# Performance work log

Hardware: AMD Instinct MI355X
Metric: run time of the kernel (lower is better)

Reference implementation:

```python
import jax, jax.numpy as jnp
import numpy as np

B, T, CIN, HID, OUT, H, W = 8, 8, 128, 64, 64, 32, 32


def _conv(x, w, b):
    # x: [B, C, H, W], w: [O, C, kh, kw] -> SAME-padded conv, stride 1
    y = jax.lax.conv_general_dilated(x, w, (1, 1), "SAME",
                                     dimension_numbers=("NCHW", "OIHW", "NCHW"))
    return y + b[None, :, None, None]


def _layer_dir(xs, w_ih, w_hh, b_ih, b_hh, reverse):
    # xs: [T, B, C, H, W]; one direction of a ConvLSTM layer; returns hs [T, B, HID, H, W]
    b, hh_, ww_ = xs.shape[1], xs.shape[3], xs.shape[4]
    h0 = jnp.zeros((b, HID, hh_, ww_), xs.dtype)

    def step(carry, x):
        h, c = carry
        gates = _conv(x, w_ih, b_ih) + _conv(h, w_hh, b_hh)  # [B, 4*HID, H, W]
        i, f, g, o = jnp.split(gates, 4, axis=1)
        c = jax.nn.sigmoid(f) * c + jax.nn.sigmoid(i) * jnp.tanh(g)
        h = jax.nn.sigmoid(o) * jnp.tanh(c)
        return (h, c), h

    _, hs = jax.lax.scan(step, (h0, h0), xs, reverse=reverse)
    return hs


def _forward(features, w_ih0f, w_hh0f, b_ih0f, b_hh0f,
             w_ih0r, w_hh0r, b_ih0r, b_hh0r,
             w_ih1f, w_hh1f, b_ih1f, b_hh1f,
             w_ih1r, w_hh1r, b_ih1r, b_hh1r,
             w_out, b_out):
    xs = jnp.transpose(features, (1, 0, 2, 3, 4))  # [T, B, C, H, W]
    # layer 0, both directions (scan reverse=True aligns outputs to original time order)
    hf = _layer_dir(xs, w_ih0f, w_hh0f, b_ih0f, b_hh0f, False)
    hr = _layer_dir(xs, w_ih0r, w_hh0r, b_ih0r, b_hh0r, True)
    xs1 = jnp.concatenate([hf, hr], axis=2)  # [T, B, 2*HID, H, W] (dropout is identity at eval)
    # layer 1
    hf1 = _layer_dir(xs1, w_ih1f, w_hh1f, b_ih1f, b_hh1f, False)
    hr1 = _layer_dir(xs1, w_ih1r, w_hh1r, b_ih1r, b_hh1r, True)
    last = jnp.concatenate([hf1[-1], hr1[-1]], axis=1)  # output[:, -1] -> [B, 2*HID, H, W]
    return jax.nn.relu(_conv(last, w_out, b_out))


def setup_inputs() -> dict:
    key = jax.random.key(0)
    ks = jax.random.split(key, 24)
    G = 4 * HID
    p = lambda k, s: jax.random.normal(k, s, jnp.float32) * 0.05
    d = {"features": jax.random.normal(ks[0], (B, T, CIN, H, W), jnp.float32)}
    i = 1
    for l, cin in ((0, CIN), (1, 2 * HID)):
        for dr in ("f", "r"):
            d[f"w_ih{l}{dr}"] = p(ks[i], (G, cin, 3, 3)); i += 1
            d[f"w_hh{l}{dr}"] = p(ks[i], (G, HID, 3, 3)); i += 1
            d[f"b_ih{l}{dr}"] = p(ks[i], (G,)); i += 1
            d[f"b_hh{l}{dr}"] = p(ks[i], (G,)); i += 1
    d["w_out"] = p(ks[i], (OUT, 2 * HID, 1, 1)); i += 1
    d["b_out"] = p(ks[i], (OUT,))
    return d


def reference(features, w_ih0f, w_hh0f, b_ih0f, b_hh0f,
              w_ih0r, w_hh0r, b_ih0r, b_hh0r,
              w_ih1f, w_hh1f, b_ih1f, b_hh1f,
              w_ih1r, w_hh1r, b_ih1r, b_hh1r,
              w_out, b_out):
    return _forward(features, w_ih0f, w_hh0f, b_ih0f, b_hh0f,
                    w_ih0r, w_hh0r, b_ih0r, b_hh0r,
                    w_ih1f, w_hh1f, b_ih1f, b_hh1f,
                    w_ih1r, w_hh1r, b_ih1r, b_hh1r,
                    w_out, b_out)
```

## Files before the change

kernel.cpp:

```cpp
#include <hip/hip_runtime.h>
#include <math.h>
#include <stdint.h>


typedef __attribute__((ext_vector_type(8))) short short8;
typedef __attribute__((ext_vector_type(4))) float float4v;

namespace {
constexpr int IMG = 34 * 34 * 64;
constexpr size_t SLOTI = 16ull * IMG;
constexpr int ROWB = 34 * 128;
constexpr int PADB = 8192;
}
template <int N> struct IC { static constexpr int v = N; };

__device__ __forceinline__ uint16_t bf16_rne(float x) {
  uint32_t u = __builtin_bit_cast(uint32_t, x);
  return (uint16_t)((u + 0x7FFFu + ((u >> 16) & 1u)) >> 16);
}
__device__ __forceinline__ float bf16_to_f(uint16_t h) {
  uint32_t u = ((uint32_t)h) << 16;
  return __builtin_bit_cast(float, u);
}

__device__ __forceinline__ void gl_lds16(const void* g, void* l) {
  __builtin_amdgcn_global_load_lds(
      (const __attribute__((address_space(1))) void*)g,
      (__attribute__((address_space(3))) void*)l, 16, 0, 0);
}

__global__ void pack_features(const float* __restrict__ f, uint16_t* __restrict__ out) {
  const size_t i = (size_t)blockIdx.x * 256 + threadIdx.x;
  const int blk_s = (int)(i & 7);
  size_t pp = i >> 3;
  const int px = (int)(pp % 34); pp /= 34;
  const int yy = (int)(pp % 34); pp /= 34;
  const int cg = (int)(pp & 3);
  const int bt = (int)(pp >> 2);
  const int b = bt & 7, t = bt >> 3;
  const int blk = blk_s ^ (px & 7);
  const int pl = blk >> 2, kg = blk & 3;
  short8 sv;
  if (px == 0 || px == 33 || yy == 0 || yy == 33) {
    #pragma unroll
    for (int j = 0; j < 8; ++j) sv[j] = 0;
  } else {
    const int x = px - 1, y = yy - 1;
    #pragma unroll
    for (int j = 0; j < 8; ++j) {
      const int ch = cg * 32 + kg * 8 + j;
      const float fv = f[(((size_t)b * 8 + t) * 128 + ch) * 1024 + y * 32 + x];
      const uint16_t hi = bf16_rne(fv);
      sv[j] = (short)(pl ? bf16_rne(fv - bf16_to_f(hi)) : hi);
    }
  }
  *(short8*)(out + i * 8) = sv;
}

struct WPackArgs {
  const float* wih[4]; const float* whh[4];
  const float* bih[4]; const float* bhh[4];
  uint32_t* wp; float* bp;
};
__global__ void pack_weights(WPackArgs A) {
  const int combo = blockIdx.y;
  const int idx = blockIdx.x * 256 + threadIdx.x;
  const int q = idx & 4095;
  const int rest = idx >> 12;
  const int nt = rest & 1;
  const int ct = rest >> 1;
  const int tap = ct % 9, cg = ct / 9;
  const int w2 = q & 3;
  const int b8s = (q >> 2) & 7;
  const int hcp = (q >> 5) & 15;
  const int g = (q >> 9) & 3;
  const int pl = (q >> 11) & 1;
  const int b8 = b8s ^ (hcp & 7);
  const int kg = b8 & 3;
  const int hcl = hcp * 2 + (b8 >> 2);
  const int n = g * 64 + nt * 32 + hcl;
  const float* wih = A.wih[combo];
  const float* whh = A.whh[combo];
  uint32_t out = 0;
  #pragma unroll
  for (int e = 0; e < 2; ++e) {
    const int ch = cg * 32 + kg * 8 + w2 * 2 + e;
    const float wv = (ch < 128) ? wih[((size_t)n * 128 + ch) * 9 + tap]
                                : whh[((size_t)n * 64 + (ch - 128)) * 9 + tap];
    const uint16_t hi = bf16_rne(wv);
    const uint16_t v = pl ? bf16_rne(wv - bf16_to_f(hi)) : hi;
    out |= ((uint32_t)v) << (16 * e);
  }
  A.wp[(size_t)combo * 442368 + idx] = out;
  if (idx < 256) A.bp[combo * 256 + idx] = A.bih[combo][idx] + A.bhh[combo][idx];
}

struct StepArgs {
  const uint16_t* in0; const uint16_t* in1; const uint16_t* in2;
  int nc0, nc1, nc2;
  const uint32_t* W;
  const float* bias;
  float* cbuf;
  uint16_t* himg;
  float* hf32;
};

__global__ __launch_bounds__(512, 2) void conv_lstm_step(StepArgs A0, StepArgs A1) {
  extern __shared__ char smem[];
  char* Asm_ = smem;
  char* Wsm_ = smem + 65536;

  const StepArgs a = (blockIdx.z == 0) ? A0 : A1;
  const int bx = blockIdx.x;
  const int nt = bx & 1;
  const int band = (bx >> 1) & 7;
  const int b = bx >> 4;
  const int y0 = band * 4;
  const int tid = threadIdx.x;
  const int lane = tid & 63;
  const int w = tid >> 6;
  const int m15 = lane & 15;
  const int kg = lane >> 4;
  const int r = w & 3;
  const int hcg = w >> 2;

  int offA[2][3][2];
  #pragma unroll
  for (int xh = 0; xh < 2; ++xh)
    #pragma unroll
    for (int kx = 0; kx < 3; ++kx)
      #pragma unroll
      for (int pl = 0; pl < 2; ++pl) {
        const int px = xh * 16 + kx + m15;
        const int sw = (pl * 4 + kg) ^ (px & 7);
        offA[xh][kx][pl] = r * ROWB + px * 128 + sw * 16;
      }
  int offW[2][4];
  {
    const int hcp = hcg * 8 + (m15 >> 1);
    const int b8 = kg + 4 * (m15 & 1);
    #pragma unroll
    for (int pl = 0; pl < 2; ++pl)
      #pragma unroll
      for (int g = 0; g < 4; ++g)
        offW[pl][g] = (((pl * 4 + g) * 16 + hcp) * 8 + (b8 ^ (hcp & 7))) * 16;
  }

  const int ncg = a.nc0 + a.nc1 + a.nc2;
  auto abase = [&](int cg) -> const char* {
    const uint16_t* t;
    if (cg < a.nc0) t = a.in0 + ((size_t)b * a.nc0 + cg) * IMG;
    else if (cg < a.nc0 + a.nc1) t = a.in1 + ((size_t)b * a.nc1 + (cg - a.nc0)) * IMG;
    else t = a.in2 + ((size_t)b * a.nc2 + (cg - a.nc0 - a.nc1)) * IMG;
    return (const char*)t + (size_t)y0 * ROWB;
  };
  auto stageA = [&](int cgi, int par) {
    const char* g = abase(cgi);
    char* d = Asm_ + par * 32768;
    #pragma unroll
    for (int j = 0; j < 4; ++j)
      gl_lds16(g + (size_t)(4 * w + j) * 1024 + lane * 16, d + (4 * w + j) * 1024);
  };
  auto stageW = [&](int cgs, int taps, int slot) {
    const char* g = (const char*)a.W + ((size_t)((cgs * 9 + taps) * 2 + nt) << 14);
    char* d = Wsm_ + slot * 16384;
    #pragma unroll
    for (int j = 0; j < 2; ++j)
      gl_lds16(g + (size_t)(2 * w + j) * 1024 + lane * 16, d + (2 * w + j) * 1024);
  };

  float4v acc[2][4];
  #pragma unroll
  for (int xh = 0; xh < 2; ++xh)
    #pragma unroll
    for (int g = 0; g < 4; ++g) acc[xh][g] = (float4v){0.f, 0.f, 0.f, 0.f};

  stageA(0, 0);
  stageW(0, 0, 0);
  stageW(0, 1, 1);

  for (int cg = 0; cg < ncg; ++cg) {
    auto tap_body = [&](auto tapc) {
      constexpr int TAP = decltype(tapc)::v;
      constexpr int CNT = (TAP == 1 || TAP == 2) ? 6 : 2;
      asm volatile("s_waitcnt vmcnt(%0)\n\ts_barrier" :: "n"(CNT) : "memory");
      const int lin = cg * 9 + TAP;
      {
        const int l2 = lin + 2;
        int cgs = l2 / 9;
        const int taps = l2 % 9;
        if (cgs >= ncg) cgs = 0;
        stageW(cgs, taps, l2 % 3);
      }
      if (TAP == 0) {
        const int nx = (cg + 1 < ncg) ? cg + 1 : 0;
        stageA(nx, (cg + 1) & 1);
      }
      constexpr int ky = TAP / 3, kx = TAP % 3;
      const char* Ab = Asm_ + (cg & 1) * 32768 + ky * ROWB;
      const char* Wb = Wsm_ + (lin % 3) * 16384;
      short8 af[2][2];
      #pragma unroll
      for (int xh = 0; xh < 2; ++xh)
        #pragma unroll
        for (int pl = 0; pl < 2; ++pl)
          af[xh][pl] = *(const short8*)(Ab + offA[xh][kx][pl]);
      short8 wfr[2][4];
      #pragma unroll
      for (int pl = 0; pl < 2; ++pl)
        #pragma unroll
        for (int g = 0; g < 4; ++g)
          wfr[pl][g] = *(const short8*)(Wb + offW[pl][g]);
      #pragma unroll
      for (int xh = 0; xh < 2; ++xh)
        #pragma unroll
        for (int g = 0; g < 4; ++g) {
          acc[xh][g] = __builtin_amdgcn_mfma_f32_16x16x32_bf16(af[xh][0], wfr[0][g], acc[xh][g], 0, 0, 0);
          acc[xh][g] = __builtin_amdgcn_mfma_f32_16x16x32_bf16(af[xh][0], wfr[1][g], acc[xh][g], 0, 0, 0);
          acc[xh][g] = __builtin_amdgcn_mfma_f32_16x16x32_bf16(af[xh][1], wfr[0][g], acc[xh][g], 0, 0, 0);
        }
    };
    tap_body(IC<0>{}); tap_body(IC<1>{}); tap_body(IC<2>{});
    tap_body(IC<3>{}); tap_body(IC<4>{}); tap_body(IC<5>{});
    tap_body(IC<6>{}); tap_body(IC<7>{}); tap_body(IC<8>{});
  }
  asm volatile("s_waitcnt vmcnt(0)" ::: "memory");

  const int hcl = hcg * 16 + m15;
  const int hc = nt * 32 + hcl;
  const int y = y0 + r;
  float bi[4];
  #pragma unroll
  for (int g = 0; g < 4; ++g) bi[g] = a.bias[g * 64 + hc];
  float* crow = a.cbuf + ((size_t)(b * 64 + hc)) * 1024 + y * 32;
  float* hrow = a.hf32 ? a.hf32 + ((size_t)(b * 64 + hc)) * 1024 + y * 32 : nullptr;
  uint16_t* hb = a.himg ? a.himg + ((size_t)(b * 2 + nt)) * IMG : nullptr;
  const int kgb = hcl >> 3, jj = hcl & 7;
  #pragma unroll
  for (int xh = 0; xh < 2; ++xh) {
    const int x0 = xh * 16 + kg * 4;
    float4v cv = *(float4v*)(crow + x0);
    float4v cn, hn;
    #pragma unroll
    for (int q = 0; q < 4; ++q) {
      const float ig = 1.f / (1.f + expf(-(acc[xh][0][q] + bi[0])));
      const float fg = 1.f / (1.f + expf(-(acc[xh][1][q] + bi[1])));
      const float gg = tanhf(acc[xh][2][q] + bi[2]);
      const float og = 1.f / (1.f + expf(-(acc[xh][3][q] + bi[3])));
      const float c2 = fg * cv[q] + ig * gg;
      cn[q] = c2;
      hn[q] = og * tanhf(c2);
    }
    *(float4v*)(crow + x0) = cn;
    if (hrow) *(float4v*)(hrow + x0) = hn;
    if (hb) {
      #pragma unroll
      for (int q = 0; q < 4; ++q) {
        const int px = x0 + q + 1;
        const int sw = px & 7;
        const uint16_t hi = bf16_rne(hn[q]);
        const uint16_t lo = bf16_rne(hn[q] - bf16_to_f(hi));
        const size_t p16 = ((size_t)(y + 1) * 34 + px) * 64;
        hb[p16 + (size_t)(kgb ^ sw) * 8 + jj] = hi;
        hb[p16 + (size_t)((4 + kgb) ^ sw) * 8 + jj] = lo;
      }
    }
  }
  if (hb) {
    {
      const int rr = tid >> 7;
      const int hlf = (tid >> 6) & 1;
      const int jx = tid & 63;
      hb[((size_t)(y0 + 1 + rr) * 34 + hlf * 33) * 64 + jx] = 0;
    }
    if (band == 0) for (int i = tid; i < 2176; i += 512) hb[i] = 0;
    if (band == 7) for (int i = tid; i < 2176; i += 512) hb[(size_t)33 * 2176 + i] = 0;
  }
}

__global__ void final_conv(const float* __restrict__ h1f_last, const float* __restrict__ h1r_last,
                           const float* __restrict__ wout, const float* __restrict__ bout,
                           float* __restrict__ out) {
  __shared__ float Ws[16 * 128];
  const int oq = blockIdx.y;
  for (int i = threadIdx.x; i < 16 * 128; i += 256) Ws[i] = wout[oq * 16 * 128 + i];
  __syncthreads();
  const int gp = blockIdx.x * 256 + threadIdx.x;
  const int b = gp >> 10, p = gp & 1023;
  float acc[16];
  #pragma unroll
  for (int o = 0; o < 16; ++o) acc[o] = bout[oq * 16 + o];
  for (int c = 0; c < 128; ++c) {
    const float xv = (c < 64) ? h1f_last[((size_t)b * 64 + c) * 1024 + p]
                              : h1r_last[((size_t)b * 64 + (c - 64)) * 1024 + p];
    #pragma unroll
    for (int o = 0; o < 16; ++o) acc[o] = fmaf(xv, Ws[o * 128 + c], acc[o]);
  }
  #pragma unroll
  for (int o = 0; o < 16; ++o) {
    const float v = acc[o];
    out[((size_t)b * 64 + oq * 16 + o) * 1024 + p] = v > 0.f ? v : 0.f;
  }
}

extern "C" void kernel_launch(void* const* d_in, const int* in_sizes, int n_in,
                              void* d_out, int out_size, void* d_ws, size_t ws_size,
                              hipStream_t stream) {
  char* p = (char*)d_ws;
  uint16_t* featImg = (uint16_t*)p; p += (size_t)8 * 8 * 4 * IMG * 2 + PADB;
  uint32_t* WP = (uint32_t*)p;      p += (size_t)4 * 442368 * 4;
  float* bp = (float*)p;            p += 4096;
  uint16_t* hf0i = (uint16_t*)p;    p += (size_t)9 * SLOTI * 2 + PADB;
  uint16_t* hr0i = (uint16_t*)p;    p += (size_t)9 * SLOTI * 2 + PADB;
  uint16_t* h1fi = (uint16_t*)p;    p += (size_t)2 * SLOTI * 2 + PADB;
  float* c0f = (float*)p;           p += (size_t)4 * 2097152;
  float* c0r = c0f + 524288;
  float* c1f = c0r + 524288;
  float* c1r = c1f + 524288;
  float* h1f8 = (float*)p;          p += 2097152;
  float* h1r8 = (float*)p;          p += 2097152;

  hipMemsetAsync(c0f, 0, (size_t)4 * 2097152, stream);
  hipMemsetAsync(hf0i, 0, (size_t)SLOTI * 2, stream);
  hipMemsetAsync(hr0i + (size_t)8 * SLOTI, 0, (size_t)SLOTI * 2, stream);
  hipMemsetAsync(h1fi, 0, (size_t)SLOTI * 2, stream);

  pack_features<<<dim3(9248), 256, 0, stream>>>((const float*)d_in[0], featImg);

  WPackArgs wa;
  for (int combo = 0; combo < 4; ++combo) {
    const int base = 1 + combo * 4;
    wa.wih[combo] = (const float*)d_in[base];
    wa.whh[combo] = (const float*)d_in[base + 1];
    wa.bih[combo] = (const float*)d_in[base + 2];
    wa.bhh[combo] = (const float*)d_in[base + 3];
  }
  wa.wp = WP; wa.bp = bp;
  pack_weights<<<dim3(1728, 4), 256, 0, stream>>>(wa);

  constexpr int DYN_LDS = 114688;
  (void)hipFuncSetAttribute((const void*)conv_lstm_step,
                            hipFuncAttributeMaxDynamicSharedMemorySize, DYN_LDS);

  auto mk = [&](const uint16_t* i0, int n0, const uint16_t* i1, int n1,
                const uint16_t* i2, int n2, int combo, float* cb,
                uint16_t* himg, float* hf32) {
    StepArgs s;
    s.in0 = i0; s.in1 = i1; s.in2 = i2;
    s.nc0 = n0; s.nc1 = n1; s.nc2 = n2;
    s.W = WP + (size_t)combo * 442368; s.bias = bp + combo * 256;
    s.cbuf = cb; s.himg = himg; s.hf32 = hf32;
    return s;
  };

  for (int k = 0; k < 8; ++k) {
    const int tr = 7 - k;
    StepArgs f = mk(featImg + (size_t)k * 8 * 4 * IMG, 4,
                    hf0i + (size_t)k * SLOTI, 2, nullptr, 0,
                    0, c0f, hf0i + (size_t)(k + 1) * SLOTI, nullptr);
    StepArgs r = mk(featImg + (size_t)tr * 8 * 4 * IMG, 4,
                    hr0i + (size_t)(tr + 1) * SLOTI, 2, nullptr, 0,
                    1, c0r, hr0i + (size_t)tr * SLOTI, nullptr);
    conv_lstm_step<<<dim3(128, 1, 2), 512, DYN_LDS, stream>>>(f, r);
  }

  for (int t = 0; t < 8; ++t) {
    uint16_t* himg = (t < 7) ? h1fi + (size_t)((t + 1) & 1) * SLOTI : nullptr;
    float* hf32 = (t == 7) ? h1f8 : nullptr;
    StepArgs s = mk(hf0i + (size_t)(t + 1) * SLOTI, 2, hr0i + (size_t)t * SLOTI, 2,
                    h1fi + (size_t)(t & 1) * SLOTI, 2, 2, c1f, himg, hf32);
    if (t == 0) {
      StepArgs rv = mk(hf0i + (size_t)8 * SLOTI, 2, hr0i + (size_t)7 * SLOTI, 2,
                       nullptr, 0, 3, c1r, nullptr, h1r8);
      conv_lstm_step<<<dim3(128, 1, 2), 512, DYN_LDS, stream>>>(s, rv);
    } else {
      conv_lstm_step<<<dim3(128, 1, 1), 512, DYN_LDS, stream>>>(s, s);
    }
  }

  final_conv<<<dim3(32, 4), 256, 0, stream>>>(
      h1f8, h1r8, (const float*)d_in[17], (const float*)d_in[18], (float*)d_out);
}
```

Before: 745.8 us.

## Double-buffer LDS fragment reads in registers and deepen weight staging ring

The inner tap loop now reads the next tap's A and W fragments from shared memory into registers while the MFMAs for the current tap run, which hides LDS read latency behind matrix work. To keep that read safe, weight staging moves from a 3-slot to a 4-slot ring with a three-tap lookahead, and dynamic LDS grows to 128 KB. The cost is about twice the fragment registers, which risks spills under the 512-thread launch bound. The larger shared-memory footprint may also limit blocks per CU.

```diff
diff --git a/kernel.cpp b/kernel.cpp
--- a/kernel.cpp
+++ b/kernel.cpp
@@ -105,6 +105,8 @@
   float* hf32;
 };
 
+struct Frags { short8 a[2][2]; short8 w[2][4]; };
+
 __global__ __launch_bounds__(512, 2) void conv_lstm_step(StepArgs A0, StepArgs A1) {
   extern __shared__ char smem[];
   char* Asm_ = smem;
@@ -168,6 +170,24 @@
     for (int j = 0; j < 2; ++j)
       gl_lds16(g + (size_t)(2 * w + j) * 1024 + lane * 16, d + (2 * w + j) * 1024);
   };
+  auto read_frags = [&](auto tapc, int cgn, int lin1) -> Frags {
+    constexpr int TN = decltype(tapc)::v;
+    constexpr int ky = TN / 3, kx = TN % 3;
+    Frags f;
+    const char* Ab = Asm_ + (cgn & 1) * 32768 + ky * ROWB;
+    const char* Wb = Wsm_ + (lin1 & 3) * 16384;
+    #pragma unroll
+    for (int xh = 0; xh < 2; ++xh)
+      #pragma unroll
+      for (int pl = 0; pl < 2; ++pl)
+        f.a[xh][pl] = *(const short8*)(Ab + offA[xh][kx][pl]);
+    #pragma unroll
+    for (int pl = 0; pl < 2; ++pl)
+      #pragma unroll
+      for (int g = 0; g < 4; ++g)
+        f.w[pl][g] = *(const short8*)(Wb + offW[pl][g]);
+    return f;
+  };
 
   float4v acc[2][4];
   #pragma unroll
@@ -178,6 +198,9 @@
   stageA(0, 0);
   stageW(0, 0, 0);
   stageW(0, 1, 1);
+  stageW(0, 2, 2);
+  asm volatile("s_waitcnt vmcnt(2)\n\ts_barrier" ::: "memory");
+  Frags cur = read_frags(IC<0>{}, 0, 0);
 
   for (int cg = 0; cg < ncg; ++cg) {
     auto tap_body = [&](auto tapc) {
@@ -186,39 +209,27 @@
       asm volatile("s_waitcnt vmcnt(%0)\n\ts_barrier" :: "n"(CNT) : "memory");
       const int lin = cg * 9 + TAP;
       {
-        const int l2 = lin + 2;
-        int cgs = l2 / 9;
-        const int taps = l2 % 9;
+        const int l3 = lin + 3;
+        int cgs = l3 / 9;
+        const int taps = l3 % 9;
         if (cgs >= ncg) cgs = 0;
-        stageW(cgs, taps, l2 % 3);
+        stageW(cgs, taps, l3 & 3);
       }
       if (TAP == 0) {
         const int nx = (cg + 1 < ncg) ? cg + 1 : 0;
         stageA(nx, (cg + 1) & 1);
       }
-      constexpr int ky = TAP / 3, kx = TAP % 3;
-      const char* Ab = Asm_ + (cg & 1) * 32768 + ky * ROWB;
-      const char* Wb = Wsm_ + (lin % 3) * 16384;
-      short8 af[2][2];
-      #pragma unroll
-      for (int xh = 0; xh < 2; ++xh)
-        #pragma unroll
-        for (int pl = 0; pl < 2; ++pl)
-          af[xh][pl] = *(const short8*)(Ab + offA[xh][kx][pl]);
-      short8 wfr[2][4];
-      #pragma unroll
-      for (int pl = 0; pl < 2; ++pl)
-        #pragma unroll
-        for (int g = 0; g < 4; ++g)
-          wfr[pl][g] = *(const short8*)(Wb + offW[pl][g]);
+      constexpr int TN = (TAP + 1) % 9;
+      Frags nxt = read_frags(IC<TN>{}, cg + (TAP == 8 ? 1 : 0), lin + 1);
       #pragma unroll
       for (int xh = 0; xh < 2; ++xh)
         #pragma unroll
         for (int g = 0; g < 4; ++g) {
-          acc[xh][g] = __builtin_amdgcn_mfma_f32_16x16x32_bf16(af[xh][0], wfr[0][g], acc[xh][g], 0, 0, 0);
-          acc[xh][g] = __builtin_amdgcn_mfma_f32_16x16x32_bf16(af[xh][0], wfr[1][g], acc[xh][g], 0, 0, 0);
-          acc[xh][g] = __builtin_amdgcn_mfma_f32_16x16x32_bf16(af[xh][1], wfr[0][g], acc[xh][g], 0, 0, 0);
+          acc[xh][g] = __builtin_amdgcn_mfma_f32_16x16x32_bf16(cur.a[xh][0], cur.w[0][g], acc[xh][g], 0, 0, 0);
+          acc[xh][g] = __builtin_amdgcn_mfma_f32_16x16x32_bf16(cur.a[xh][0], cur.w[1][g], acc[xh][g], 0, 0, 0);
+          acc[xh][g] = __builtin_amdgcn_mfma_f32_16x16x32_bf16(cur.a[xh][1], cur.w[0][g], acc[xh][g], 0, 0, 0);
         }
+      cur = nxt;
     };
     tap_body(IC<0>{}); tap_body(IC<1>{}); tap_body(IC<2>{});
     tap_body(IC<3>{}); tap_body(IC<4>{}); tap_body(IC<5>{});
@@ -338,7 +349,7 @@
   wa.wp = WP; wa.bp = bp;
   pack_weights<<<dim3(1728, 4), 256, 0, stream>>>(wa);
 
-  constexpr int DYN_LDS = 114688;
+  constexpr int DYN_LDS = 131072;
   (void)hipFuncSetAttribute((const void*)conv_lstm_step,
                             hipFuncAttributeMaxDynamicSharedMemorySize, DYN_LDS);
 
```

Measured after the change: 773.9 us. +3.8%, slower.
